# Performance work log

Hardware: AMD Instinct MI355X
Metric: run time of the kernel (lower is better)

## Reference

```python
import jax, jax.numpy as jnp
import numpy as np

B, TQ, TK, D, H = 2, 2048, 2048, 1024, 16
HD = D // H
MLP = 4 * D
EPS = 1e-5


def _ln(x, g, b):
    m = jnp.mean(x, axis=-1, keepdims=True)
    v = jnp.mean(jnp.square(x - m), axis=-1, keepdims=True)
    return (x - m) * jax.lax.rsqrt(v + EPS) * g + b


def setup_inputs() -> dict:
    key = jax.random.key(0)
    ks = jax.random.split(key, 16)
    s = 0.02
    inp = {
        "x": jax.random.normal(ks[0], (B, TQ, D), jnp.float32),
        "enc_out": jax.random.normal(ks[1], (B, TK, D), jnp.float32),
        "causal_mask": jnp.tril(jnp.ones((TQ, TQ), jnp.int32)),
        # LayerNorm params
        "ln1_g": jnp.ones((D,), jnp.float32), "ln1_b": jnp.zeros((D,), jnp.float32),
        "ln2_g": jnp.ones((D,), jnp.float32), "ln2_b": jnp.zeros((D,), jnp.float32),
        "ln3_g": jnp.ones((D,), jnp.float32), "ln3_b": jnp.zeros((D,), jnp.float32),
        # self-attn (weights stored [in, out])
        "qkv_w": jax.random.normal(ks[2], (D, 3 * D), jnp.float32) * s,
        "qkv_b": jnp.zeros((3 * D,), jnp.float32),
        "proj_w": jax.random.normal(ks[3], (D, D), jnp.float32) * s,
        "proj_b": jnp.zeros((D,), jnp.float32),
        # cross-attn
        "q_w": jax.random.normal(ks[4], (D, D), jnp.float32) * s,
        "q_b": jnp.zeros((D,), jnp.float32),
        "kv_w": jax.random.normal(ks[5], (D, 2 * D), jnp.float32) * s,
        "kv_b": jnp.zeros((2 * D,), jnp.float32),
        "co_w": jax.random.normal(ks[6], (D, D), jnp.float32) * s,
        "co_b": jnp.zeros((D,), jnp.float32),
        # MLP
        "mlp1_w": jax.random.normal(ks[7], (D, MLP), jnp.float32) * s,
        "mlp1_b": jnp.zeros((MLP,), jnp.float32),
        "mlp2_w": jax.random.normal(ks[8], (MLP, D), jnp.float32) * s,
        "mlp2_b": jnp.zeros((D,), jnp.float32),
    }
    return inp


def _self_attn(x, mask, qkv_w, qkv_b, proj_w, proj_b):
    b, t, d = x.shape
    qkv = (x @ qkv_w + qkv_b).reshape(b, t, 3, H, HD)
    q, k, v = qkv[:, :, 0], qkv[:, :, 1], qkv[:, :, 2]  # [b,t,H,HD]
    scale = HD ** (-0.5)
    attn = jnp.einsum('bqhd,bkhd->bhqk', q, k) * scale
    attn = jnp.where(mask[None, None] == 0, -jnp.inf, attn)
    attn = jax.nn.softmax(attn, axis=-1)
    out = jnp.einsum('bhqk,bkhd->bqhd', attn, v).reshape(b, t, d)
    return out @ proj_w + proj_b


def _cross_attn(q_in, kv_in, q_w, q_b, kv_w, kv_b, co_w, co_b):
    b, tq, d = q_in.shape
    tk = kv_in.shape[1]
    Q = (q_in @ q_w + q_b).reshape(b, tq, H, HD)
    KV = (kv_in @ kv_w + kv_b).reshape(b, tk, 2, H, HD)
    K, V = KV[:, :, 0], KV[:, :, 1]
    scale = HD ** (-0.5)
    attn = jnp.einsum('bqhd,bkhd->bhqk', Q, K) * scale
    attn = jax.nn.softmax(attn, axis=-1)
    out = jnp.einsum('bhqk,bkhd->bqhd', attn, V).reshape(b, tq, d)
    return out @ co_w + co_b


def reference(x, enc_out, causal_mask, ln1_g, ln1_b, ln2_g, ln2_b, ln3_g, ln3_b,
              qkv_w, qkv_b, proj_w, proj_b, q_w, q_b, kv_w, kv_b, co_w, co_b,
              mlp1_w, mlp1_b, mlp2_w, mlp2_b):
    x = x + _self_attn(_ln(x, ln1_g, ln1_b), causal_mask, qkv_w, qkv_b, proj_w, proj_b)
    x = x + _cross_attn(_ln(x, ln2_g, ln2_b), enc_out, q_w, q_b, kv_w, kv_b, co_w, co_b)
    h = _ln(x, ln3_g, ln3_b)
    h = jax.nn.gelu(h @ mlp1_w + mlp1_b, approximate=False) @ mlp2_w + mlp2_b
    return x + h
```

## Files before the change

kernel.cpp:

```cpp
#include <hip/hip_runtime.h>
#include <hip/hip_bf16.h>
#include <cstdint>
#include <cstddef>


#define DEV __device__ __forceinline__

typedef short bf16x8 __attribute__((ext_vector_type(8)));
typedef float f32x4  __attribute__((ext_vector_type(4)));

DEV unsigned short f2bf(float f) {
  unsigned int u = __builtin_bit_cast(unsigned int, f);
  u = u + 0x7FFFu + ((u >> 16) & 1u);
  return (unsigned short)(u >> 16);
}

DEV void gload_lds16(const void* g, void* lds) {
  __builtin_amdgcn_global_load_lds(
      (const __attribute__((address_space(1))) void*)g,
      (__attribute__((address_space(3))) void*)lds, 16, 0, 0);
}

__global__ __launch_bounds__(256) void k_transpose_bf16(
    const float* __restrict__ in, unsigned short* __restrict__ out, int K, int N) {
  __shared__ float tile[32][33];
  const int n0 = blockIdx.x * 32, k0 = blockIdx.y * 32;
  const int tx = threadIdx.x, ty = threadIdx.y;
#pragma unroll
  for (int i = 0; i < 32; i += 8)
    tile[ty + i][tx] = in[(size_t)(k0 + ty + i) * N + n0 + tx];
  __syncthreads();
#pragma unroll
  for (int i = 0; i < 32; i += 8)
    out[(size_t)(n0 + ty + i) * K + k0 + tx] = f2bf(tile[tx][ty + i]);
}

__global__ __launch_bounds__(256) void k_vtrans(
    const unsigned short* __restrict__ V, int ldv, int vo0,
    unsigned short* __restrict__ vt, int TK) {
  __shared__ unsigned short tile[32][33];
  const int k0 = blockIdx.x * 32;
  const int d0 = (blockIdx.y & 1) * 32;
  const int bh = blockIdx.z;
  const int b = bh >> 4, h = bh & 15;
  const int tx = threadIdx.x, ty = threadIdx.y;
  const size_t tok0 = (size_t)b * 2048;
#pragma unroll
  for (int i = 0; i < 32; i += 8)
    tile[ty + i][tx] = V[(tok0 + k0 + ty + i) * ldv + vo0 + h * 64 + d0 + tx];
  __syncthreads();
#pragma unroll
  for (int i = 0; i < 32; i += 8)
    vt[((size_t)bh * 64 + d0 + ty + i) * TK + k0 + tx] = tile[tx][ty + i];
}

__global__ __launch_bounds__(256) void k_f32_to_bf16(
    const float* __restrict__ in, unsigned short* __restrict__ out, int n4) {
  const int i = blockIdx.x * 256 + threadIdx.x;
  if (i < n4) {
    const float4 v = ((const float4*)in)[i];
    ushort4 o;
    o.x = f2bf(v.x); o.y = f2bf(v.y); o.z = f2bf(v.z); o.w = f2bf(v.w);
    ((ushort4*)out)[i] = o;
  }
}

__global__ __launch_bounds__(256) void k_ln(
    const float* __restrict__ x, const float* __restrict__ g,
    const float* __restrict__ bt, unsigned short* __restrict__ y) {
  const int row = blockIdx.x, t = threadIdx.x;
  const float4 v = ((const float4*)(x + (size_t)row * 1024))[t];
  float s1 = v.x + v.y + v.z + v.w;
  float s2 = v.x * v.x + v.y * v.y + v.z * v.z + v.w * v.w;
#pragma unroll
  for (int off = 1; off < 64; off <<= 1) {
    s1 += __shfl_xor(s1, off);
    s2 += __shfl_xor(s2, off);
  }
  __shared__ float r1[4], r2[4];
  if ((t & 63) == 0) { r1[t >> 6] = s1; r2[t >> 6] = s2; }
  __syncthreads();
  const float tot1 = r1[0] + r1[1] + r1[2] + r1[3];
  const float tot2 = r2[0] + r2[1] + r2[2] + r2[3];
  const float mean = tot1 * (1.0f / 1024.0f);
  const float var  = tot2 * (1.0f / 1024.0f) - mean * mean;
  const float rstd = rsqrtf(var + 1e-5f);
  const float4 gg = ((const float4*)g)[t];
  const float4 bb = ((const float4*)bt)[t];
  ushort4 o;
  o.x = f2bf((v.x - mean) * rstd * gg.x + bb.x);
  o.y = f2bf((v.y - mean) * rstd * gg.y + bb.y);
  o.z = f2bf((v.z - mean) * rstd * gg.z + bb.z);
  o.w = f2bf((v.w - mean) * rstd * gg.w + bb.w);
  ((ushort4*)(y + (size_t)row * 1024))[t] = o;
}

template <int EPI>
__global__ __launch_bounds__(256) void k_gemm(
    const unsigned short* __restrict__ A, const unsigned short* __restrict__ Bt,
    const float* __restrict__ bias, const float* __restrict__ resid,
    unsigned short* __restrict__ Obf, float* __restrict__ Of, int N, int K) {
  __shared__ __align__(16) unsigned short As[128 * 32];
  __shared__ __align__(16) unsigned short Bs[128 * 32];
  const int tid = threadIdx.x;
  const int wave = tid >> 6, lane = tid & 63;
  const int bm = blockIdx.y, bn = blockIdx.x;
  const int la = lane & 15, ks = (lane >> 4) * 8;
  const int wr = wave >> 1, wc = wave & 1;
  f32x4 acc[4][4] = {};
  const int r0 = wave * 32 + (lane >> 2);
  const int kk = (lane & 3) * 8;
  const unsigned short* ga = A  + (size_t)(bm * 128 + r0) * K + kk;
  const unsigned short* gb = Bt + (size_t)(bn * 128 + r0) * K + kk;
  unsigned short* lA0 = &As[(wave * 32) * 32];
  unsigned short* lA1 = &As[(wave * 32 + 16) * 32];
  unsigned short* lB0 = &Bs[(wave * 32) * 32];
  unsigned short* lB1 = &Bs[(wave * 32 + 16) * 32];
  for (int kt = 0; kt < K; kt += 32) {
    gload_lds16(ga + kt,                  lA0);
    gload_lds16(ga + kt + (size_t)16 * K, lA1);
    gload_lds16(gb + kt,                  lB0);
    gload_lds16(gb + kt + (size_t)16 * K, lB1);
    __syncthreads();
    bf16x8 af[4], bfr[4];
#pragma unroll
    for (int m = 0; m < 4; ++m)
      af[m] = *(const bf16x8*)&As[(wr * 64 + m * 16 + la) * 32 + ks];
#pragma unroll
    for (int n = 0; n < 4; ++n)
      bfr[n] = *(const bf16x8*)&Bs[(wc * 64 + n * 16 + la) * 32 + ks];
#pragma unroll
    for (int m = 0; m < 4; ++m)
#pragma unroll
      for (int n = 0; n < 4; ++n)
        acc[m][n] = __builtin_amdgcn_mfma_f32_16x16x32_bf16(af[m], bfr[n], acc[m][n], 0, 0, 0);
    __syncthreads();
  }
#pragma unroll
  for (int m = 0; m < 4; ++m) {
    const int row = bm * 128 + wr * 64 + m * 16 + (lane >> 4) * 4;
#pragma unroll
    for (int n = 0; n < 4; ++n) {
      const int col = bn * 128 + wc * 64 + n * 16 + la;
      const float bv = bias[col];
#pragma unroll
      for (int r = 0; r < 4; ++r) {
        float v = acc[m][n][r] + bv;
        const size_t idx = (size_t)(row + r) * N + col;
        if constexpr (EPI == 0) {
          Obf[idx] = f2bf(v);
        } else if constexpr (EPI == 1) {
          Of[idx] = v + resid[idx];
        } else {
          v = 0.5f * v * (1.0f + erff(v * 0.70710678118654752f));
          Obf[idx] = f2bf(v);
        }
      }
    }
  }
}

template <bool CAUSAL>
__global__ __launch_bounds__(256) void k_attn2(
    const unsigned short* __restrict__ Qb, int ldq, int qo0,
    const unsigned short* __restrict__ Kb, int ldk, int ko0,
    const unsigned short* __restrict__ Vtg,
    unsigned short* __restrict__ O, int TK) {
  __shared__ __align__(16) unsigned short Ks[2][64 * 64];
  __shared__ __align__(16) unsigned short Vs[2][64 * 64];
  __shared__ __align__(16) unsigned short Pl[4][16 * 64];
  const int qt = blockIdx.x, h = blockIdx.y, b = blockIdx.z;
  const int bh = b * 16 + h;
  const int tid = threadIdx.x, wave = tid >> 6, lane = tid & 63;
  const int la = lane & 15, ks8 = (lane >> 4) * 8;
  const int qoff = qo0 + h * 64, koff = ko0 + h * 64;
  const size_t tok0 = (size_t)b * 2048;

  bf16x8 qf[2];
  {
    const unsigned short* qp =
        Qb + (tok0 + qt * 64 + wave * 16 + la) * ldq + qoff + ks8;
    qf[0] = *(const bf16x8*)qp;
    qf[1] = *(const bf16x8*)(qp + 32);
  }
  f32x4 oacc[4] = {};
  float m_r[4], l_r[4];
#pragma unroll
  for (int r = 0; r < 4; ++r) { m_r[r] = -1e30f; l_r[r] = 0.0f; }

  const int nkt = CAUSAL ? (qt + 1) : (TK >> 6);

  const int rr = lane >> 3, cc = lane & 7;
  const int sc = (cc ^ rr) * 8;
  const unsigned short* Vrow = Vtg + (size_t)bh * 64 * TK;
  auto stage = [&](int kt, int buf) {
#pragma unroll
    for (int r = 0; r < 2; ++r) {
      const int row = wave * 8 + r * 32 + rr;
      gload_lds16(Kb + (tok0 + kt * 64 + row) * ldk + koff + sc,
                  &Ks[buf][(wave * 8 + r * 32) * 64]);
      gload_lds16(Vrow + (size_t)row * TK + kt * 64 + sc,
                  &Vs[buf][(wave * 8 + r * 32) * 64]);
    }
  };

  stage(0, 0);
  int cur = 0;
  unsigned short* pw = Pl[wave];
  const int lsw = (la & 7) << 4;

  for (int kt = 0; kt < nkt; ++kt) {
    if (kt + 1 < nkt) {
      stage(kt + 1, cur ^ 1);
      asm volatile("s_waitcnt vmcnt(4)" ::: "memory");
    } else {
      asm volatile("s_waitcnt vmcnt(0)" ::: "memory");
    }
    __syncthreads();

    f32x4 s[4] = {};
#pragma unroll
    for (int kc = 0; kc < 2; ++kc)
#pragma unroll
      for (int n = 0; n < 4; ++n) {
        const int key = n * 16 + la;
        const bf16x8 bfrag = *(const bf16x8*)((const char*)&Ks[cur][0] +
            key * 128 + ((kc * 64 + ks8 * 2) ^ ((key & 7) << 4)));
        s[n] = __builtin_amdgcn_mfma_f32_16x16x32_bf16(qf[kc], bfrag, s[n], 0, 0, 0);
      }

    float alpha[4], p[4][4];
#pragma unroll
    for (int r = 0; r < 4; ++r) {
      float x0 = s[0][r] * 0.125f, x1 = s[1][r] * 0.125f;
      float x2 = s[2][r] * 0.125f, x3 = s[3][r] * 0.125f;
      if (CAUSAL && kt == nkt - 1) {
        const int qloc = wave * 16 + (lane >> 4) * 4 + r;
        if (0 * 16 + la > qloc) x0 = -1e30f;
        if (1 * 16 + la > qloc) x1 = -1e30f;
        if (2 * 16 + la > qloc) x2 = -1e30f;
        if (3 * 16 + la > qloc) x3 = -1e30f;
      }
      float tm = fmaxf(fmaxf(x0, x1), fmaxf(x2, x3));
      tm = fmaxf(tm, __shfl_xor(tm, 1, 16));
      tm = fmaxf(tm, __shfl_xor(tm, 2, 16));
      tm = fmaxf(tm, __shfl_xor(tm, 4, 16));
      tm = fmaxf(tm, __shfl_xor(tm, 8, 16));
      const float mn = fmaxf(m_r[r], tm);
      alpha[r] = __expf(m_r[r] - mn);
      m_r[r] = mn;
      const float e0 = __expf(x0 - mn), e1 = __expf(x1 - mn);
      const float e2 = __expf(x2 - mn), e3 = __expf(x3 - mn);
      float rs = (e0 + e1) + (e2 + e3);
      rs += __shfl_xor(rs, 1, 16);
      rs += __shfl_xor(rs, 2, 16);
      rs += __shfl_xor(rs, 4, 16);
      rs += __shfl_xor(rs, 8, 16);
      l_r[r] = l_r[r] * alpha[r] + rs;
      p[0][r] = e0; p[1][r] = e1; p[2][r] = e2; p[3][r] = e3;
    }
#pragma unroll
    for (int n4 = 0; n4 < 4; ++n4)
#pragma unroll
      for (int r = 0; r < 4; ++r) oacc[n4][r] *= alpha[r];

#pragma unroll
    for (int r = 0; r < 4; ++r) {
      const int qr = (lane >> 4) * 4 + r;
      char* prow = (char*)pw + qr * 128;
      const int swz = (qr & 7) << 4;
#pragma unroll
      for (int n = 0; n < 4; ++n)
        *(unsigned short*)(prow + ((n * 32 + la * 2) ^ swz)) = f2bf(p[n][r]);
    }
    asm volatile("s_waitcnt lgkmcnt(0)" ::: "memory");
    bf16x8 pa[2];
    pa[0] = *(const bf16x8*)((const char*)pw + la * 128 + ((ks8 * 2) ^ lsw));
    pa[1] = *(const bf16x8*)((const char*)pw + la * 128 + ((64 + ks8 * 2) ^ lsw));

#pragma unroll
    for (int kc = 0; kc < 2; ++kc)
#pragma unroll
      for (int n4 = 0; n4 < 4; ++n4) {
        const int d = n4 * 16 + la;
        const bf16x8 vb = *(const bf16x8*)((const char*)&Vs[cur][0] +
            d * 128 + ((kc * 64 + ks8 * 2) ^ ((d & 7) << 4)));
        oacc[n4] = __builtin_amdgcn_mfma_f32_16x16x32_bf16(pa[kc], vb, oacc[n4], 0, 0, 0);
      }
    __syncthreads();
    cur ^= 1;
  }

  const size_t orow0 = tok0 + qt * 64 + wave * 16 + (lane >> 4) * 4;
  const int ocol0 = h * 64;
#pragma unroll
  for (int n4 = 0; n4 < 4; ++n4)
#pragma unroll
    for (int r = 0; r < 4; ++r)
      O[(orow0 + r) * 1024 + ocol0 + n4 * 16 + la] = f2bf(oacc[n4][r] / l_r[r]);
}

constexpr size_t SZ_1K1K  = 1024ull * 1024 * 2;
constexpr size_t OFF_WQKV = 0;                         constexpr size_t SZ_WQKV = 3072ull * 1024 * 2;
constexpr size_t OFF_WPRJ = OFF_WQKV + SZ_WQKV;
constexpr size_t OFF_WQ   = OFF_WPRJ + SZ_1K1K;
constexpr size_t OFF_WKV  = OFF_WQ + SZ_1K1K;          constexpr size_t SZ_WKV = 2048ull * 1024 * 2;
constexpr size_t OFF_WCO  = OFF_WKV + SZ_WKV;
constexpr size_t OFF_WM1  = OFF_WCO + SZ_1K1K;         constexpr size_t SZ_WM1 = 4096ull * 1024 * 2;
constexpr size_t OFF_WM2  = OFF_WM1 + SZ_WM1;          constexpr size_t SZ_WM2 = 1024ull * 4096 * 2;
constexpr size_t OFF_ENCB = OFF_WM2 + SZ_WM2;          constexpr size_t SZ_ACT = 4096ull * 1024 * 2;
constexpr size_t OFF_XCUR = OFF_ENCB + SZ_ACT;         constexpr size_t SZ_XF  = 4096ull * 1024 * 4;
constexpr size_t OFF_LNO  = OFF_XCUR + SZ_XF;
constexpr size_t OFF_BIG  = OFF_LNO + SZ_ACT;          constexpr size_t SZ_BIG = 4096ull * 4096 * 2;
constexpr size_t OFF_ATTN = OFF_BIG + SZ_BIG;
constexpr size_t OFF_QPRJ = OFF_ATTN + SZ_ACT;
constexpr size_t WS_NEED  = OFF_QPRJ + SZ_ACT;

extern "C" void kernel_launch(void* const* d_in, const int* in_sizes, int n_in,
                              void* d_out, int out_size, void* d_ws, size_t ws_size,
                              hipStream_t stream) {
  (void)in_sizes; (void)n_in; (void)out_size;
  if (ws_size < WS_NEED) return;

  const float* x     = (const float*)d_in[0];
  const float* enc   = (const float*)d_in[1];
  const float* ln1g  = (const float*)d_in[3];
  const float* ln1b  = (const float*)d_in[4];
  const float* ln2g  = (const float*)d_in[5];
  const float* ln2b  = (const float*)d_in[6];
  const float* ln3g  = (const float*)d_in[7];
  const float* ln3b  = (const float*)d_in[8];
  const float* qkv_w = (const float*)d_in[9];
  const float* qkv_b = (const float*)d_in[10];
  const float* prj_w = (const float*)d_in[11];
  const float* prj_b = (const float*)d_in[12];
  const float* q_w   = (const float*)d_in[13];
  const float* q_b   = (const float*)d_in[14];
  const float* kv_w  = (const float*)d_in[15];
  const float* kv_b  = (const float*)d_in[16];
  const float* co_w  = (const float*)d_in[17];
  const float* co_b  = (const float*)d_in[18];
  const float* m1_w  = (const float*)d_in[19];
  const float* m1_b  = (const float*)d_in[20];
  const float* m2_w  = (const float*)d_in[21];
  const float* m2_b  = (const float*)d_in[22];
  float* out = (float*)d_out;

  char* ws = (char*)d_ws;
  unsigned short* wqkv = (unsigned short*)(ws + OFF_WQKV);
  unsigned short* wprj = (unsigned short*)(ws + OFF_WPRJ);
  unsigned short* wq   = (unsigned short*)(ws + OFF_WQ);
  unsigned short* wkv  = (unsigned short*)(ws + OFF_WKV);
  unsigned short* wco  = (unsigned short*)(ws + OFF_WCO);
  unsigned short* wm1  = (unsigned short*)(ws + OFF_WM1);
  unsigned short* wm2  = (unsigned short*)(ws + OFF_WM2);
  unsigned short* encb = (unsigned short*)(ws + OFF_ENCB);
  float*          xcur = (float*)(ws + OFF_XCUR);
  unsigned short* lno  = (unsigned short*)(ws + OFF_LNO);
  unsigned short* big  = (unsigned short*)(ws + OFF_BIG);
  unsigned short* attnb= (unsigned short*)(ws + OFF_ATTN);
  unsigned short* qprj = (unsigned short*)(ws + OFF_QPRJ);
  unsigned short* vtS  = big + (size_t)4096 * 3072;
  unsigned short* vtC  = big + (size_t)4096 * 2048;

  const dim3 tb(32, 8);
  k_transpose_bf16<<<dim3(3072/32, 1024/32), tb, 0, stream>>>(qkv_w, wqkv, 1024, 3072);
  k_transpose_bf16<<<dim3(1024/32, 1024/32), tb, 0, stream>>>(prj_w, wprj, 1024, 1024);
  k_transpose_bf16<<<dim3(1024/32, 1024/32), tb, 0, stream>>>(q_w,   wq,   1024, 1024);
  k_transpose_bf16<<<dim3(2048/32, 1024/32), tb, 0, stream>>>(kv_w,  wkv,  1024, 2048);
  k_transpose_bf16<<<dim3(1024/32, 1024/32), tb, 0, stream>>>(co_w,  wco,  1024, 1024);
  k_transpose_bf16<<<dim3(4096/32, 1024/32), tb, 0, stream>>>(m1_w,  wm1,  1024, 4096);
  k_transpose_bf16<<<dim3(1024/32, 4096/32), tb, 0, stream>>>(m2_w,  wm2,  4096, 1024);
  k_f32_to_bf16<<<4096, 256, 0, stream>>>(enc, encb, 1048576);

  k_ln<<<4096, 256, 0, stream>>>(x, ln1g, ln1b, lno);
  k_gemm<0><<<dim3(24, 32), 256, 0, stream>>>(lno, wqkv, qkv_b, nullptr, big, nullptr, 3072, 1024);
  k_vtrans<<<dim3(64, 2, 32), tb, 0, stream>>>(big, 3072, 2048, vtS, 2048);
  k_attn2<true><<<dim3(32, 16, 2), 256, 0, stream>>>(big, 3072, 0,
                                                     big, 3072, 1024,
                                                     vtS, attnb, 2048);
  k_gemm<1><<<dim3(8, 32), 256, 0, stream>>>(attnb, wprj, prj_b, x, nullptr, xcur, 1024, 1024);

  k_ln<<<4096, 256, 0, stream>>>(xcur, ln2g, ln2b, lno);
  k_gemm<0><<<dim3(8, 32), 256, 0, stream>>>(lno,  wq,  q_b,  nullptr, qprj, nullptr, 1024, 1024);
  k_gemm<0><<<dim3(16, 32), 256, 0, stream>>>(encb, wkv, kv_b, nullptr, big,  nullptr, 2048, 1024);
  k_vtrans<<<dim3(64, 2, 32), tb, 0, stream>>>(big, 2048, 1024, vtC, 2048);
  k_attn2<false><<<dim3(32, 16, 2), 256, 0, stream>>>(qprj, 1024, 0,
                                                      big,  2048, 0,
                                                      vtC, attnb, 2048);
  k_gemm<1><<<dim3(8, 32), 256, 0, stream>>>(attnb, wco, co_b, xcur, nullptr, xcur, 1024, 1024);

  k_ln<<<4096, 256, 0, stream>>>(xcur, ln3g, ln3b, lno);
  k_gemm<2><<<dim3(32, 32), 256, 0, stream>>>(lno, wm1, m1_b, nullptr, big, nullptr, 4096, 1024);
  k_gemm<1><<<dim3(8, 32), 256, 0, stream>>>(big, wm2, m2_b, xcur, nullptr, out, 1024, 4096);
}
```

Before: 763.6 us.

## Transpose attention MFMA layout, use exp2 softmax, swizzle GEMM and attention block order

Rewrites the flash-attention kernel to compute S^T (K as A operand), so each lane owns one query row. The row max and sum then need only two cross-lane shuffles instead of eight per row. It also folds log2(e) into the scale to use exp2f, packs P writes as 32-bit stores, and stages the output through LDS for 16-byte coalesced global stores. It adds s_setprio around the MFMA sections, rotates q-tile assignment per head to balance causal work, and swizzles the GEMM workgroup order for better L2 locality. These are several interacting changes that carry layout-correctness risk.

```diff
diff --git a/kernel.cpp b/kernel.cpp
--- a/kernel.cpp
+++ b/kernel.cpp
@@ -104,7 +104,10 @@
   __shared__ __align__(16) unsigned short Bs[128 * 32];
   const int tid = threadIdx.x;
   const int wave = tid >> 6, lane = tid & 63;
-  const int bm = blockIdx.y, bn = blockIdx.x;
+  const int nwg = gridDim.x * gridDim.y;
+  const int wg = blockIdx.y * gridDim.x + blockIdx.x;
+  const int swz = (wg & 7) * (nwg >> 3) + (wg >> 3);
+  const int bn = swz % gridDim.x, bm = swz / gridDim.x;
   const int la = lane & 15, ks = (lane >> 4) * 8;
   const int wr = wave >> 1, wc = wave & 1;
   f32x4 acc[4][4] = {};
@@ -161,7 +164,7 @@
 }
 
 template <bool CAUSAL>
-__global__ __launch_bounds__(256) void k_attn2(
+__global__ __launch_bounds__(256) void k_attn3(
     const unsigned short* __restrict__ Qb, int ldq, int qo0,
     const unsigned short* __restrict__ Kb, int ldk, int ko0,
     const unsigned short* __restrict__ Vtg,
@@ -169,24 +172,24 @@
   __shared__ __align__(16) unsigned short Ks[2][64 * 64];
   __shared__ __align__(16) unsigned short Vs[2][64 * 64];
   __shared__ __align__(16) unsigned short Pl[4][16 * 64];
-  const int qt = blockIdx.x, h = blockIdx.y, b = blockIdx.z;
+  const int qt = (blockIdx.x + blockIdx.y) & 31;
+  const int h = blockIdx.y, b = blockIdx.z;
   const int bh = b * 16 + h;
   const int tid = threadIdx.x, wave = tid >> 6, lane = tid & 63;
-  const int la = lane & 15, ks8 = (lane >> 4) * 8;
+  const int la = lane & 15, g = lane >> 4;
   const int qoff = qo0 + h * 64, koff = ko0 + h * 64;
   const size_t tok0 = (size_t)b * 2048;
+  constexpr float SCALE = 0.125f * 1.44269504088896f;
 
   bf16x8 qf[2];
   {
     const unsigned short* qp =
-        Qb + (tok0 + qt * 64 + wave * 16 + la) * ldq + qoff + ks8;
+        Qb + (tok0 + qt * 64 + wave * 16 + la) * ldq + qoff + g * 8;
     qf[0] = *(const bf16x8*)qp;
     qf[1] = *(const bf16x8*)(qp + 32);
   }
   f32x4 oacc[4] = {};
-  float m_r[4], l_r[4];
-#pragma unroll
-  for (int r = 0; r < 4; ++r) { m_r[r] = -1e30f; l_r[r] = 0.0f; }
+  float m_r = -1e30f, l_r = 0.0f;
 
   const int nkt = CAUSAL ? (qt + 1) : (TK >> 6);
 
@@ -206,7 +209,7 @@
 
   stage(0, 0);
   int cur = 0;
-  unsigned short* pw = Pl[wave];
+  char* pw = (char*)Pl[wave];
   const int lsw = (la & 7) << 4;
 
   for (int kt = 0; kt < nkt; ++kt) {
@@ -216,88 +219,108 @@
     } else {
       asm volatile("s_waitcnt vmcnt(0)" ::: "memory");
     }
-    __syncthreads();
+    __builtin_amdgcn_s_barrier();
 
     f32x4 s[4] = {};
+    __builtin_amdgcn_s_setprio(1);
 #pragma unroll
     for (int kc = 0; kc < 2; ++kc)
 #pragma unroll
       for (int n = 0; n < 4; ++n) {
         const int key = n * 16 + la;
-        const bf16x8 bfrag = *(const bf16x8*)((const char*)&Ks[cur][0] +
-            key * 128 + ((kc * 64 + ks8 * 2) ^ ((key & 7) << 4)));
-        s[n] = __builtin_amdgcn_mfma_f32_16x16x32_bf16(qf[kc], bfrag, s[n], 0, 0, 0);
+        const bf16x8 kfr = *(const bf16x8*)((const char*)&Ks[cur][0] +
+            key * 128 + ((kc * 64 + g * 16) ^ ((key & 7) << 4)));
+        s[n] = __builtin_amdgcn_mfma_f32_16x16x32_bf16(kfr, qf[kc], s[n], 0, 0, 0);
       }
-
-    float alpha[4], p[4][4];
-#pragma unroll
-    for (int r = 0; r < 4; ++r) {
-      float x0 = s[0][r] * 0.125f, x1 = s[1][r] * 0.125f;
-      float x2 = s[2][r] * 0.125f, x3 = s[3][r] * 0.125f;
-      if (CAUSAL && kt == nkt - 1) {
-        const int qloc = wave * 16 + (lane >> 4) * 4 + r;
-        if (0 * 16 + la > qloc) x0 = -1e30f;
-        if (1 * 16 + la > qloc) x1 = -1e30f;
-        if (2 * 16 + la > qloc) x2 = -1e30f;
-        if (3 * 16 + la > qloc) x3 = -1e30f;
+    __builtin_amdgcn_s_setprio(0);
+
+    float xx[4][4];
+#pragma unroll
+    for (int n = 0; n < 4; ++n)
+#pragma unroll
+      for (int r = 0; r < 4; ++r) xx[n][r] = s[n][r] * SCALE;
+    if (CAUSAL && kt == nkt - 1) {
+      const int qloc = wave * 16 + la;
+#pragma unroll
+      for (int n = 0; n < 4; ++n)
+#pragma unroll
+        for (int r = 0; r < 4; ++r)
+          if (n * 16 + g * 4 + r > qloc) xx[n][r] = -1e30f;
+    }
+    float t0 = fmaxf(fmaxf(xx[0][0], xx[0][1]), fmaxf(xx[0][2], xx[0][3]));
+    float t1 = fmaxf(fmaxf(xx[1][0], xx[1][1]), fmaxf(xx[1][2], xx[1][3]));
+    float t2 = fmaxf(fmaxf(xx[2][0], xx[2][1]), fmaxf(xx[2][2], xx[2][3]));
+    float t3 = fmaxf(fmaxf(xx[3][0], xx[3][1]), fmaxf(xx[3][2], xx[3][3]));
+    float tm = fmaxf(fmaxf(t0, t1), fmaxf(t2, t3));
+    tm = fmaxf(tm, __shfl_xor(tm, 16, 64));
+    tm = fmaxf(tm, __shfl_xor(tm, 32, 64));
+    const float mn = fmaxf(m_r, tm);
+    const float al = exp2f(m_r - mn);
+    m_r = mn;
+    float p[4][4];
+#pragma unroll
+    for (int n = 0; n < 4; ++n)
+#pragma unroll
+      for (int r = 0; r < 4; ++r) p[n][r] = exp2f(xx[n][r] - mn);
+    float rs = ((p[0][0] + p[0][1]) + (p[0][2] + p[0][3]))
+             + ((p[1][0] + p[1][1]) + (p[1][2] + p[1][3]))
+             + ((p[2][0] + p[2][1]) + (p[2][2] + p[2][3]))
+             + ((p[3][0] + p[3][1]) + (p[3][2] + p[3][3]));
+    rs += __shfl_xor(rs, 16, 64);
+    rs += __shfl_xor(rs, 32, 64);
+    l_r = l_r * al + rs;
+#pragma unroll
+    for (int n4 = 0; n4 < 4; ++n4)
+#pragma unroll
+      for (int r = 0; r < 4; ++r) oacc[n4][r] *= al;
+
+#pragma unroll
+    for (int n = 0; n < 4; ++n)
+#pragma unroll
+      for (int rp = 0; rp < 2; ++rp) {
+        const unsigned int w = (unsigned int)f2bf(p[n][2 * rp]) |
+                               ((unsigned int)f2bf(p[n][2 * rp + 1]) << 16);
+        *(unsigned int*)(pw + la * 128 + ((n * 32 + g * 8 + rp * 4) ^ lsw)) = w;
       }
-      float tm = fmaxf(fmaxf(x0, x1), fmaxf(x2, x3));
-      tm = fmaxf(tm, __shfl_xor(tm, 1, 16));
-      tm = fmaxf(tm, __shfl_xor(tm, 2, 16));
-      tm = fmaxf(tm, __shfl_xor(tm, 4, 16));
-      tm = fmaxf(tm, __shfl_xor(tm, 8, 16));
-      const float mn = fmaxf(m_r[r], tm);
-      alpha[r] = __expf(m_r[r] - mn);
-      m_r[r] = mn;
-      const float e0 = __expf(x0 - mn), e1 = __expf(x1 - mn);
-      const float e2 = __expf(x2 - mn), e3 = __expf(x3 - mn);
-      float rs = (e0 + e1) + (e2 + e3);
-      rs += __shfl_xor(rs, 1, 16);
-      rs += __shfl_xor(rs, 2, 16);
-      rs += __shfl_xor(rs, 4, 16);
-      rs += __shfl_xor(rs, 8, 16);
-      l_r[r] = l_r[r] * alpha[r] + rs;
-      p[0][r] = e0; p[1][r] = e1; p[2][r] = e2; p[3][r] = e3;
-    }
-#pragma unroll
-    for (int n4 = 0; n4 < 4; ++n4)
-#pragma unroll
-      for (int r = 0; r < 4; ++r) oacc[n4][r] *= alpha[r];
-
-#pragma unroll
-    for (int r = 0; r < 4; ++r) {
-      const int qr = (lane >> 4) * 4 + r;
-      char* prow = (char*)pw + qr * 128;
-      const int swz = (qr & 7) << 4;
-#pragma unroll
-      for (int n = 0; n < 4; ++n)
-        *(unsigned short*)(prow + ((n * 32 + la * 2) ^ swz)) = f2bf(p[n][r]);
-    }
     asm volatile("s_waitcnt lgkmcnt(0)" ::: "memory");
-    bf16x8 pa[2];
-    pa[0] = *(const bf16x8*)((const char*)pw + la * 128 + ((ks8 * 2) ^ lsw));
-    pa[1] = *(const bf16x8*)((const char*)pw + la * 128 + ((64 + ks8 * 2) ^ lsw));
-
+    bf16x8 pb[2];
+    pb[0] = *(const bf16x8*)(pw + la * 128 + ((0 * 64 + g * 16) ^ lsw));
+    pb[1] = *(const bf16x8*)(pw + la * 128 + ((1 * 64 + g * 16) ^ lsw));
+
+    __builtin_amdgcn_s_setprio(1);
 #pragma unroll
     for (int kc = 0; kc < 2; ++kc)
 #pragma unroll
       for (int n4 = 0; n4 < 4; ++n4) {
         const int d = n4 * 16 + la;
         const bf16x8 vb = *(const bf16x8*)((const char*)&Vs[cur][0] +
-            d * 128 + ((kc * 64 + ks8 * 2) ^ ((d & 7) << 4)));
-        oacc[n4] = __builtin_amdgcn_mfma_f32_16x16x32_bf16(pa[kc], vb, oacc[n4], 0, 0, 0);
+            d * 128 + ((kc * 64 + g * 16) ^ ((d & 7) << 4)));
+        oacc[n4] = __builtin_amdgcn_mfma_f32_16x16x32_bf16(vb, pb[kc], oacc[n4], 0, 0, 0);
       }
-    __syncthreads();
+    __builtin_amdgcn_s_setprio(0);
+    asm volatile("s_waitcnt lgkmcnt(0)" ::: "memory");
+    __builtin_amdgcn_s_barrier();
     cur ^= 1;
   }
 
-  const size_t orow0 = tok0 + qt * 64 + wave * 16 + (lane >> 4) * 4;
-  const int ocol0 = h * 64;
+  const float inv = 1.0f / l_r;
 #pragma unroll
   for (int n4 = 0; n4 < 4; ++n4)
 #pragma unroll
-    for (int r = 0; r < 4; ++r)
-      O[(orow0 + r) * 1024 + ocol0 + n4 * 16 + la] = f2bf(oacc[n4][r] / l_r[r]);
+    for (int rp = 0; rp < 2; ++rp) {
+      const unsigned int w = (unsigned int)f2bf(oacc[n4][2 * rp] * inv) |
+                             ((unsigned int)f2bf(oacc[n4][2 * rp + 1] * inv) << 16);
+      *(unsigned int*)(pw + la * 128 + ((n4 * 32 + g * 8 + rp * 4) ^ lsw)) = w;
+    }
+  asm volatile("s_waitcnt lgkmcnt(0)" ::: "memory");
+  const int q2 = lane >> 2, c4 = lane & 3;
+  const size_t orow = tok0 + qt * 64 + wave * 16 + q2;
+#pragma unroll
+  for (int h8 = 0; h8 < 2; ++h8) {
+    const bf16x8 v = *(const bf16x8*)(pw + q2 * 128 +
+        ((c4 * 32 + h8 * 16) ^ ((q2 & 7) << 4)));
+    *(bf16x8*)&O[orow * 1024 + h * 64 + c4 * 16 + h8 * 8] = v;
+  }
 }
 
 constexpr size_t SZ_1K1K  = 1024ull * 1024 * 2;
@@ -376,7 +399,7 @@
   k_ln<<<4096, 256, 0, stream>>>(x, ln1g, ln1b, lno);
   k_gemm<0><<<dim3(24, 32), 256, 0, stream>>>(lno, wqkv, qkv_b, nullptr, big, nullptr, 3072, 1024);
   k_vtrans<<<dim3(64, 2, 32), tb, 0, stream>>>(big, 3072, 2048, vtS, 2048);
-  k_attn2<true><<<dim3(32, 16, 2), 256, 0, stream>>>(big, 3072, 0,
+  k_attn3<true><<<dim3(32, 16, 2), 256, 0, stream>>>(big, 3072, 0,
                                                      big, 3072, 1024,
                                                      vtS, attnb, 2048);
   k_gemm<1><<<dim3(8, 32), 256, 0, stream>>>(attnb, wprj, prj_b, x, nullptr, xcur, 1024, 1024);
@@ -385,7 +408,7 @@
   k_gemm<0><<<dim3(8, 32), 256, 0, stream>>>(lno,  wq,  q_b,  nullptr, qprj, nullptr, 1024, 1024);
   k_gemm<0><<<dim3(16, 32), 256, 0, stream>>>(encb, wkv, kv_b, nullptr, big,  nullptr, 2048, 1024);
   k_vtrans<<<dim3(64, 2, 32), tb, 0, stream>>>(big, 2048, 1024, vtC, 2048);
-  k_attn2<false><<<dim3(32, 16, 2), 256, 0, stream>>>(qprj, 1024, 0,
+  k_attn3<false><<<dim3(32, 16, 2), 256, 0, stream>>>(qprj, 1024, 0,
                                                       big,  2048, 0,
                                                       vtC, attnb, 2048);
   k_gemm<1><<<dim3(8, 32), 256, 0, stream>>>(attnb, wco, co_b, xcur, nullptr, xcur, 1024, 1024);
```

New measurement: 692.9 us. 1.1x faster.
